# Performance work log

Hardware: AMD Instinct MI355X
Metric: run time of the kernel (lower is better)

The kernel has to match this reference:

```python
import jax, jax.numpy as jnp
import numpy as np

B, S, D, H, L, DFF, WIN = 2, 2048, 768, 12, 2, 3072, 512
EPS = 1e-5
DH = D // H


def setup_inputs() -> dict:
    key = jax.random.key(0)
    ks = jax.random.split(key, 8)
    rn = lambda k, shape: jax.random.normal(k, shape, jnp.float32) * 0.02
    inp = {
        "src": jax.random.normal(ks[0], (B, S, D), jnp.float32),
        "qw": rn(ks[1], (L, D, D)), "qb": jnp.zeros((L, D), jnp.float32),
        "kw": rn(ks[2], (L, D, D)), "kb": jnp.zeros((L, D), jnp.float32),
        "vw": rn(ks[3], (L, D, D)), "vb": jnp.zeros((L, D), jnp.float32),
        "ow": rn(ks[4], (L, D, D)), "ob": jnp.zeros((L, D), jnp.float32),
        "w1": rn(ks[5], (L, DFF, D)), "b1": jnp.zeros((L, DFF), jnp.float32),
        "w2": rn(ks[6], (L, D, DFF)), "b2": jnp.zeros((L, D), jnp.float32),
        "g1": jnp.ones((L, D), jnp.float32), "be1": jnp.zeros((L, D), jnp.float32),
        "g2": jnp.ones((L, D), jnp.float32), "be2": jnp.zeros((L, D), jnp.float32),
    }
    return inp


def _ln(x, g, b):
    m = jnp.mean(x, axis=-1, keepdims=True)
    v = jnp.mean(jnp.square(x - m), axis=-1, keepdims=True)
    return (x - m) * jax.lax.rsqrt(v + EPS) * g + b


def _encoder(src, qw, qb, kw, kb, vw, vb, ow, ob, w1, b1, w2, b2, g1, be1, g2, be2):
    scale = DH ** -0.5
    idx = jnp.arange(S)
    # non-causal sliding window: |i - j| <= window_size // 2
    band = jnp.abs(idx[:, None] - idx[None, :]) <= (WIN // 2)
    neg = -jnp.finfo(jnp.float32).max
    x = src
    for l in range(L):
        # projections -> (B, H, S, DH)
        q = (x @ qw[l].T + qb[l]).reshape(B, S, H, DH).transpose(0, 2, 1, 3)
        k = (x @ kw[l].T + kb[l]).reshape(B, S, H, DH).transpose(0, 2, 1, 3)
        v = (x @ vw[l].T + vb[l]).reshape(B, S, H, DH).transpose(0, 2, 1, 3)
        # full dense scores then band mask (faithful to the original module)
        sim = jnp.einsum('bhid,bhjd->bhij', q * scale, k)
        sim = jnp.where(band, sim, neg)
        attn = jax.nn.softmax(sim, axis=-1)
        o = jnp.einsum('bhij,bhjd->bhid', attn, v)
        o = o.transpose(0, 2, 1, 3).reshape(B, S, D) @ ow[l].T + ob[l]
        # post-norm transformer block (norm_first=False)
        x = _ln(x + o, g1[l], be1[l])
        ff = jax.nn.relu(x @ w1[l].T + b1[l]) @ w2[l].T + b2[l]
        x = _ln(x + ff, g2[l], be2[l])
    return x


def reference(src, qw, qb, kw, kb, vw, vb, ow, ob, w1, b1, w2, b2, g1, be1, g2, be2):
    return _encoder(src, qw, qb, kw, kb, vw, vb, ow, ob, w1, b1, w2, b2, g1, be1, g2, be2)
```

## Files before the change

kernel.cpp:

```cpp
#include <hip/hip_runtime.h>
#include <math.h>

#define BATCH 2
#define SEQ   2048
#define DM    768
#define NHD   12
#define NL    2
#define DFF   3072
#define DH    64
#define HW    256
#define MR    (BATCH*SEQ)
#define EPSF  1e-5f
#define SCALE 0.125f
#define QKVS  2304

typedef __attribute__((ext_vector_type(8))) __bf16 bf16x8;
typedef __attribute__((ext_vector_type(4))) float  f32x4;

__device__ __forceinline__ ushort f2bu(float f) {
    union { __bf16 h; ushort u; } c;
    c.h = (__bf16)f;
    return c.u;
}
__device__ __forceinline__ float bu2f(ushort u) {
    union { uint u; float f; } c;
    c.u = ((uint)u) << 16;
    return c.f;
}

__device__ __forceinline__ void gload16(const ushort* g, ushort* l) {
    __builtin_amdgcn_global_load_lds(
        (const __attribute__((address_space(1))) void*)g,
        (__attribute__((address_space(3))) void*)l, 16, 0, 0);
}

__device__ __forceinline__ void xcd_swz(int& bx, int& by, int& bz) {
    const int gx = gridDim.x, gy = gridDim.y;
    const int nwg = gx * gy * gridDim.z;
    int lin = bx + gx * (by + gy * bz);
    lin = (lin & 7) * (nwg >> 3) + (lin >> 3);
    bx = lin % gx;
    int rest = lin / gx;
    by = rest % gy;
    bz = rest / gy;
}

__global__ __launch_bounds__(256) void cvt(const float* __restrict__ in,
                                           ushort* __restrict__ out, int n)
{
    int i = (blockIdx.x * 256 + threadIdx.x) * 4;
    if (i >= n) return;
    float4 v = *(const float4*)(in + i);
    ushort4 o;
    o.x = f2bu(v.x); o.y = f2bu(v.y); o.z = f2bu(v.z); o.w = f2bu(v.w);
    *(ushort4*)(out + i) = o;
}

__global__ __launch_bounds__(256) void gemm128(
    const ushort* __restrict__ A, const ushort* __restrict__ W,
    const float* __restrict__ bias, ushort* __restrict__ C,
    int M, int N, int K, int relu)
{
    __shared__ ushort As[2][128 * 32];
    __shared__ ushort Ws[2][128 * 32];

    int bxi = blockIdx.x, byi = blockIdx.y, bzi = blockIdx.z;
    xcd_swz(bxi, byi, bzi);

    const int t  = threadIdx.x;
    const int bm = byi * 128;
    const int bn = bxi * 128;

    const int w    = t >> 6;
    const int lane = t & 63;
    const int quad = lane >> 4;
    const int lrow = lane & 15;
    const int wm   = (w >> 1) * 64;
    const int wn   = (w & 1) * 64;

    const int srow = t >> 2;
    const int scol = (t & 3) * 8;
    const ushort* ag = A + (size_t)(bm + srow) * K + scol;
    const ushort* wg = W + (size_t)(bn + srow) * K + scol;

    f32x4 acc[4][4] = {};

    gload16(ag,                  &As[0][t * 8]);
    gload16(ag + (size_t)64 * K, &As[0][2048 + t * 8]);
    gload16(wg,                  &Ws[0][t * 8]);
    gload16(wg + (size_t)64 * K, &Ws[0][2048 + t * 8]);
    __syncthreads();

    int cur = 0;
    for (int k0 = 0; k0 < K; k0 += 32) {
        const int nxt = cur ^ 1;
        if (k0 + 32 < K) {
            gload16(ag + k0 + 32,                  &As[nxt][t * 8]);
            gload16(ag + (size_t)64 * K + k0 + 32, &As[nxt][2048 + t * 8]);
            gload16(wg + k0 + 32,                  &Ws[nxt][t * 8]);
            gload16(wg + (size_t)64 * K + k0 + 32, &Ws[nxt][2048 + t * 8]);
        }

        bf16x8 af[4], bfr[4];
#pragma unroll
        for (int i = 0; i < 4; ++i)
            af[i] = *(const bf16x8*)&As[cur][(wm + i * 16 + lrow) * 32 + quad * 8];
#pragma unroll
        for (int j = 0; j < 4; ++j)
            bfr[j] = *(const bf16x8*)&Ws[cur][(wn + j * 16 + lrow) * 32 + quad * 8];

#pragma unroll
        for (int i = 0; i < 4; ++i)
#pragma unroll
            for (int j = 0; j < 4; ++j)
                acc[i][j] = __builtin_amdgcn_mfma_f32_16x16x32_bf16(
                    af[i], bfr[j], acc[i][j], 0, 0, 0);
        __syncthreads();
        cur = nxt;
    }

#pragma unroll
    for (int j = 0; j < 4; ++j) {
        const int col = bn + wn + j * 16 + lrow;
        const float bv = bias[col];
#pragma unroll
        for (int i = 0; i < 4; ++i) {
            const int rb = bm + wm + i * 16 + quad * 4;
#pragma unroll
            for (int r = 0; r < 4; ++r) {
                float vv = acc[i][j][r] + bv;
                if (relu) vv = fmaxf(vv, 0.f);
                C[(size_t)(rb + r) * N + col] = f2bu(vv);
            }
        }
    }
}

__global__ __launch_bounds__(256) void gemm64(
    const ushort* __restrict__ A, const ushort* __restrict__ W,
    const float* __restrict__ bias, ushort* __restrict__ C,
    float* __restrict__ part, int M, int N, int Kc, int ldk, int relu)
{
    __shared__ ushort As[2][64 * 32];
    __shared__ ushort Ws[2][128 * 32];

    int bxi = blockIdx.x, byi = blockIdx.y, bzi = blockIdx.z;
    xcd_swz(bxi, byi, bzi);

    const int t  = threadIdx.x;
    const int bm = byi * 64;
    const int bn = bxi * 128;
    const int z  = bzi;
    const int kbase = z * Kc;

    const int w    = t >> 6;
    const int lane = t & 63;
    const int quad = lane >> 4;
    const int lrow = lane & 15;
    const int wm   = (w >> 1) * 32;
    const int wn   = (w & 1) * 64;

    const int srow = t >> 2;
    const int scol = (t & 3) * 8;
    const ushort* ag = A + (size_t)(bm + srow) * ldk + kbase + scol;
    const ushort* wg = W + (size_t)(bn + srow) * ldk + kbase + scol;

    f32x4 acc[2][4] = {};

    gload16(ag,                    &As[0][t * 8]);
    gload16(wg,                    &Ws[0][t * 8]);
    gload16(wg + (size_t)64 * ldk, &Ws[0][2048 + t * 8]);
    __syncthreads();

    int cur = 0;
    for (int k0 = 0; k0 < Kc; k0 += 32) {
        const int nxt = cur ^ 1;
        if (k0 + 32 < Kc) {
            gload16(ag + k0 + 32,                    &As[nxt][t * 8]);
            gload16(wg + k0 + 32,                    &Ws[nxt][t * 8]);
            gload16(wg + (size_t)64 * ldk + k0 + 32, &Ws[nxt][2048 + t * 8]);
        }

        bf16x8 af[2], bfr[4];
#pragma unroll
        for (int i = 0; i < 2; ++i)
            af[i] = *(const bf16x8*)&As[cur][(wm + i * 16 + lrow) * 32 + quad * 8];
#pragma unroll
        for (int j = 0; j < 4; ++j)
            bfr[j] = *(const bf16x8*)&Ws[cur][(wn + j * 16 + lrow) * 32 + quad * 8];

#pragma unroll
        for (int i = 0; i < 2; ++i)
#pragma unroll
            for (int j = 0; j < 4; ++j)
                acc[i][j] = __builtin_amdgcn_mfma_f32_16x16x32_bf16(
                    af[i], bfr[j], acc[i][j], 0, 0, 0);
        __syncthreads();
        cur = nxt;
    }

    if (gridDim.z > 1) {
        float* po = part + (size_t)z * M * N;
#pragma unroll
        for (int j = 0; j < 4; ++j) {
            const int col = bn + wn + j * 16 + lrow;
#pragma unroll
            for (int i = 0; i < 2; ++i) {
                const int rb = bm + wm + i * 16 + quad * 4;
#pragma unroll
                for (int r = 0; r < 4; ++r)
                    po[(size_t)(rb + r) * N + col] = acc[i][j][r];
            }
        }
    } else {
#pragma unroll
        for (int j = 0; j < 4; ++j) {
            const int col = bn + wn + j * 16 + lrow;
            const float bv = bias[col];
#pragma unroll
            for (int i = 0; i < 2; ++i) {
                const int rb = bm + wm + i * 16 + quad * 4;
#pragma unroll
                for (int r = 0; r < 4; ++r) {
                    float vv = acc[i][j][r] + bv;
                    if (relu) vv = fmaxf(vv, 0.f);
                    C[(size_t)(rb + r) * N + col] = f2bu(vv);
                }
            }
        }
    }
}

#define QT  64
#define NCH 9
#define KP  72

__global__ __launch_bounds__(256) void attn(
    const ushort* __restrict__ q, const ushort* __restrict__ k,
    const ushort* __restrict__ v, ushort* __restrict__ o)
{
    __shared__ ushort kv[2][64][KP];
    __shared__ ushort vt[2][64][KP];
    __shared__ ushort sc[QT][KP];

    int bxi = blockIdx.x, byi = blockIdx.y, bzi = blockIdx.z;
    xcd_swz(bxi, byi, bzi);

    const int t    = threadIdx.x;
    const int i0   = bxi * QT;
    const int h    = byi;
    const int b    = bzi;
    const size_t ibase = (size_t)b * SEQ * QKVS + (size_t)h * DH;
    const size_t obase = (size_t)b * SEQ * DM   + (size_t)h * DH;

    const int w    = t >> 6;
    const int lane = t & 63;
    const int quad = lane >> 4;
    const int lrow = lane & 15;
    const int qrow = w * 16;

    const int jstart = i0 - HW;

    const int sjj[2] = { t >> 3, (t + 256) >> 3 };
    const int sd0[2] = { (t & 7) * 8, (t & 7) * 8 };

#pragma unroll
    for (int e = 0; e < 2; ++e) {
        int idx = t + 256 * e;
        int qi = idx >> 3, d0 = (idx & 7) * 8;
        uint4 raw = *(const uint4*)(q + ibase + (size_t)(i0 + qi) * QKVS + d0);
        *(uint4*)&sc[qi][d0] = raw;
    }
    uint4 kr[2], vr[2];
#pragma unroll
    for (int e = 0; e < 2; ++e) {
        int j = jstart + sjj[e];
        kr[e] = make_uint4(0, 0, 0, 0);
        vr[e] = make_uint4(0, 0, 0, 0);
        if (j >= 0 && j < SEQ) {
            kr[e] = *(const uint4*)(k + ibase + (size_t)j * QKVS + sd0[e]);
            vr[e] = *(const uint4*)(v + ibase + (size_t)j * QKVS + sd0[e]);
        }
    }
#pragma unroll
    for (int e = 0; e < 2; ++e) {
        *(uint4*)&kv[0][sjj[e]][sd0[e]] = kr[e];
        const ushort* u = (const ushort*)&vr[e];
#pragma unroll
        for (int x = 0; x < 8; ++x) {
            int dh  = sd0[e] + x;
            int blk = ((sjj[e] >> 3) ^ (dh >> 3)) & 7;
            vt[0][dh][blk * 8 + (sjj[e] & 7)] = u[x];
        }
    }
    __syncthreads();

    const bf16x8 a0 = *(const bf16x8*)&sc[qrow + lrow][quad * 8];
    const bf16x8 a1 = *(const bf16x8*)&sc[qrow + lrow][32 + quad * 8];

    float m_r[4], l_r[4];
    f32x4 oacc[4] = {};
#pragma unroll
    for (int r = 0; r < 4; ++r) { m_r[r] = -1e20f; l_r[r] = 0.f; }

    for (int c = 0; c < NCH; ++c) {
        const int cur = c & 1;
        const int j0  = jstart + c * 64;

        if (c + 1 < NCH) {
            const int j0n = jstart + (c + 1) * 64;
#pragma unroll
            for (int e = 0; e < 2; ++e) {
                int j = j0n + sjj[e];
                kr[e] = make_uint4(0, 0, 0, 0);
                vr[e] = make_uint4(0, 0, 0, 0);
                if (j >= 0 && j < SEQ) {
                    kr[e] = *(const uint4*)(k + ibase + (size_t)j * QKVS + sd0[e]);
                    vr[e] = *(const uint4*)(v + ibase + (size_t)j * QKVS + sd0[e]);
                }
            }
        }

        float p[4][4];
#pragma unroll
        for (int kt = 0; kt < 4; ++kt) {
            const int krow = kt * 16;
            bf16x8 b0 = *(const bf16x8*)&kv[cur][krow + lrow][quad * 8];
            bf16x8 b1 = *(const bf16x8*)&kv[cur][krow + lrow][32 + quad * 8];
            f32x4 acc = {};
            acc = __builtin_amdgcn_mfma_f32_16x16x32_bf16(a0, b0, acc, 0, 0, 0);
            acc = __builtin_amdgcn_mfma_f32_16x16x32_bf16(a1, b1, acc, 0, 0, 0);
            const int jg = j0 + krow + lrow;
#pragma unroll
            for (int r = 0; r < 4; ++r) {
                const int ig = i0 + qrow + quad * 4 + r;
                bool ok = (jg >= 0) && (jg < SEQ) &&
                          (jg >= ig - HW) && (jg <= ig + HW);
                p[kt][r] = ok ? acc[r] * SCALE : -1e30f;
            }
        }

#pragma unroll
        for (int r = 0; r < 4; ++r) {
            float cm = fmaxf(fmaxf(p[0][r], p[1][r]), fmaxf(p[2][r], p[3][r]));
#pragma unroll
            for (int off = 8; off; off >>= 1) cm = fmaxf(cm, __shfl_xor(cm, off));
            const float mn = fmaxf(m_r[r], cm);
            const float f  = __expf(m_r[r] - mn);
            m_r[r] = mn;
            float cs = 0.f;
#pragma unroll
            for (int kt = 0; kt < 4; ++kt) {
                float e = __expf(p[kt][r] - mn);
                p[kt][r] = e;
                cs += e;
            }
#pragma unroll
            for (int off = 8; off; off >>= 1) cs += __shfl_xor(cs, off);
            l_r[r] = l_r[r] * f + cs;
#pragma unroll
            for (int nt = 0; nt < 4; ++nt) oacc[nt][r] *= f;
        }

#pragma unroll
        for (int kt = 0; kt < 4; ++kt)
#pragma unroll
            for (int r = 0; r < 4; ++r)
                sc[qrow + quad * 4 + r][kt * 16 + lrow] = f2bu(p[kt][r]);

        bf16x8 pa0 = *(const bf16x8*)&sc[qrow + lrow][quad * 8];
        bf16x8 pa1 = *(const bf16x8*)&sc[qrow + lrow][32 + quad * 8];
#pragma unroll
        for (int nt = 0; nt < 4; ++nt) {
            const int dh  = nt * 16 + lrow;
            const int rsw = (dh >> 3) & 7;
            bf16x8 b0 = *(const bf16x8*)&vt[cur][dh][((quad)     ^ rsw) * 8];
            bf16x8 b1 = *(const bf16x8*)&vt[cur][dh][((quad + 4) ^ rsw) * 8];
            oacc[nt] = __builtin_amdgcn_mfma_f32_16x16x32_bf16(pa0, b0, oacc[nt], 0, 0, 0);
            oacc[nt] = __builtin_amdgcn_mfma_f32_16x16x32_bf16(pa1, b1, oacc[nt], 0, 0, 0);
        }

        if (c + 1 < NCH) {
            const int nxt = cur ^ 1;
#pragma unroll
            for (int e = 0; e < 2; ++e) {
                *(uint4*)&kv[nxt][sjj[e]][sd0[e]] = kr[e];
                const ushort* u = (const ushort*)&vr[e];
#pragma unroll
                for (int x = 0; x < 8; ++x) {
                    int dh  = sd0[e] + x;
                    int blk = ((sjj[e] >> 3) ^ (dh >> 3)) & 7;
                    vt[nxt][dh][blk * 8 + (sjj[e] & 7)] = u[x];
                }
            }
        }
        __syncthreads();
    }

#pragma unroll
    for (int r = 0; r < 4; ++r) {
        const float inv = 1.f / l_r[r];
        const int qi = i0 + qrow + quad * 4 + r;
#pragma unroll
        for (int nt = 0; nt < 4; ++nt)
            o[obase + (size_t)qi * DM + nt * 16 + lrow] = f2bu(oacc[nt][r] * inv);
    }
}

__global__ __launch_bounds__(256) void add_ln(
    const ushort* __restrict__ xa, const ushort* __restrict__ yb,
    const float* __restrict__ g, const float* __restrict__ be,
    ushort* __restrict__ ob, float* __restrict__ of, int fin)
{
    const int r = blockIdx.x * 4 + (threadIdx.x >> 6);
    const int t = threadIdx.x & 63;
    const size_t off = (size_t)r * DM;
    float sv[12];
    float s1 = 0.f, s2 = 0.f;
#pragma unroll
    for (int ii = 0; ii < 12; ++ii) {
        float vv = bu2f(xa[off + t + 64 * ii]) + bu2f(yb[off + t + 64 * ii]);
        sv[ii] = vv; s1 += vv; s2 += vv * vv;
    }
#pragma unroll
    for (int o2 = 32; o2; o2 >>= 1) {
        s1 += __shfl_xor(s1, o2);
        s2 += __shfl_xor(s2, o2);
    }
    const float mean = s1 * (1.f / 768.f);
    const float rstd = rsqrtf(s2 * (1.f / 768.f) - mean * mean + EPSF);
#pragma unroll
    for (int ii = 0; ii < 12; ++ii) {
        const int c = t + 64 * ii;
        float v = (sv[ii] - mean) * rstd * g[c] + be[c];
        if (fin) of[off + c] = v;
        else     ob[off + c] = f2bu(v);
    }
}

__global__ __launch_bounds__(256) void add_ln_sk(
    const ushort* __restrict__ xa, const float* __restrict__ pp,
    const float* __restrict__ bias, const float* __restrict__ g,
    const float* __restrict__ be,
    ushort* __restrict__ ob, float* __restrict__ of, int fin)
{
    const int r = blockIdx.x * 4 + (threadIdx.x >> 6);
    const int t = threadIdx.x & 63;
    const size_t off = (size_t)r * DM;
    float sv[12];
    float s1 = 0.f, s2 = 0.f;
#pragma unroll
    for (int ii = 0; ii < 12; ++ii) {
        const int c = t + 64 * ii;
        float vv = bu2f(xa[off + c]) + pp[off + c]
                 + pp[(size_t)MR * DM + off + c] + bias[c];
        sv[ii] = vv; s1 += vv; s2 += vv * vv;
    }
#pragma unroll
    for (int o2 = 32; o2; o2 >>= 1) {
        s1 += __shfl_xor(s1, o2);
        s2 += __shfl_xor(s2, o2);
    }
    const float mean = s1 * (1.f / 768.f);
    const float rstd = rsqrtf(s2 * (1.f / 768.f) - mean * mean + EPSF);
#pragma unroll
    for (int ii = 0; ii < 12; ++ii) {
        const int c = t + 64 * ii;
        float v = (sv[ii] - mean) * rstd * g[c] + be[c];
        if (fin) of[off + c] = v;
        else     ob[off + c] = f2bu(v);
    }
}

extern "C" void kernel_launch(void* const* d_in, const int* in_sizes, int n_in,
                              void* d_out, int out_size, void* d_ws, size_t ws_size,
                              hipStream_t stream) {
    (void)in_sizes; (void)n_in; (void)out_size; (void)ws_size;
    const float* src = (const float*)d_in[0];
    const float* qw  = (const float*)d_in[1];
    const float* qb  = (const float*)d_in[2];
    const float* kw  = (const float*)d_in[3];
    const float* kb  = (const float*)d_in[4];
    const float* vw  = (const float*)d_in[5];
    const float* vb  = (const float*)d_in[6];
    const float* ow  = (const float*)d_in[7];
    const float* ob  = (const float*)d_in[8];
    const float* w1  = (const float*)d_in[9];
    const float* b1  = (const float*)d_in[10];
    const float* w2  = (const float*)d_in[11];
    const float* b2  = (const float*)d_in[12];
    const float* g1  = (const float*)d_in[13];
    const float* be1 = (const float*)d_in[14];
    const float* g2  = (const float*)d_in[15];
    const float* be2 = (const float*)d_in[16];

    const size_t A    = (size_t)MR * DM;
    const size_t WD1  = (size_t)DM * DM;
    const size_t WQKV = (size_t)3 * DM * DM;
    const size_t WF1  = (size_t)DFF * DM;
    const size_t WF   = (size_t)NL * WF1;

    float*  bcat = (float*)d_ws;
    ushort* p    = (ushort*)(bcat + (size_t)NL * QKVS);
    ushort* qkvwB = p; p += (size_t)NL * WQKV;
    ushort* owB   = p; p += (size_t)NL * WD1;
    ushort* w1B   = p; p += WF;
    ushort* w2B   = p; p += WF;
    ushort* xb    = p; p += A;
    ushort* qkvB  = p; p += 3 * A;
    ushort* oB    = p; p += A;
    ushort* yB    = p; p += A;
    ushort* h1    = p; p += A;
    ushort* ffh   = p;

    float* part = (float*)qkvB;

    for (int l = 0; l < NL; ++l) {
        hipMemcpyAsync(bcat + (size_t)l * QKVS + 0,    qb + (size_t)l * DM,
                       DM * sizeof(float), hipMemcpyDeviceToDevice, stream);
        hipMemcpyAsync(bcat + (size_t)l * QKVS + DM,   kb + (size_t)l * DM,
                       DM * sizeof(float), hipMemcpyDeviceToDevice, stream);
        hipMemcpyAsync(bcat + (size_t)l * QKVS + 2*DM, vb + (size_t)l * DM,
                       DM * sizeof(float), hipMemcpyDeviceToDevice, stream);
    }

    for (int l = 0; l < NL; ++l) {
        cvt<<<(int)(WD1 / 1024), 256, 0, stream>>>(
            qw + (size_t)l * WD1, qkvwB + (size_t)l * WQKV + 0,     (int)WD1);
        cvt<<<(int)(WD1 / 1024), 256, 0, stream>>>(
            kw + (size_t)l * WD1, qkvwB + (size_t)l * WQKV + WD1,   (int)WD1);
        cvt<<<(int)(WD1 / 1024), 256, 0, stream>>>(
            vw + (size_t)l * WD1, qkvwB + (size_t)l * WQKV + 2*WD1, (int)WD1);
    }
    cvt<<<(int)(NL * WD1 / 1024), 256, 0, stream>>>(ow, owB, (int)(NL * WD1));
    cvt<<<(int)(WF / 1024), 256, 0, stream>>>(w1, w1B, (int)WF);
    cvt<<<(int)(WF / 1024), 256, 0, stream>>>(w2, w2B, (int)WF);
    cvt<<<(int)(A  / 1024), 256, 0, stream>>>(src, xb, (int)A);

    const dim3 gQKV(QKVS / 128, MR / 128);
    const dim3 gO(DM / 128, MR / 64);
    const dim3 gF1(DFF / 128, MR / 128);
    const dim3 gF2(DM / 128, MR / 64, 2);
    const dim3 gA(SEQ / QT, NHD, BATCH);

    for (int l = 0; l < NL; ++l) {
        const size_t bD = (size_t)l * DM;
        const size_t bF = (size_t)l * DFF;

        gemm128<<<gQKV, 256, 0, stream>>>(xb, qkvwB + (size_t)l * WQKV,
                                          bcat + (size_t)l * QKVS, qkvB,
                                          MR, QKVS, DM, 0);
        attn<<<gA, 256, 0, stream>>>(qkvB, qkvB + DM, qkvB + 2 * DM, oB);
        gemm64<<<gO, 256, 0, stream>>>(oB, owB + (size_t)l * WD1, ob + bD, yB,
                                       nullptr, MR, DM, DM, DM, 0);
        add_ln<<<MR / 4, 256, 0, stream>>>(xb, yB, g1 + bD, be1 + bD,
                                           h1, nullptr, 0);
        gemm128<<<gF1, 256, 0, stream>>>(h1, w1B + (size_t)l * WF1, b1 + bF, ffh,
                                         MR, DFF, DM, 1);
        gemm64<<<gF2, 256, 0, stream>>>(ffh, w2B + (size_t)l * WF1, nullptr,
                                        nullptr, part, MR, DM, DFF / 2, DFF, 0);
        if (l == NL - 1)
            add_ln_sk<<<MR / 4, 256, 0, stream>>>(h1, part, b2 + bD,
                                                  g2 + bD, be2 + bD,
                                                  nullptr, (float*)d_out, 1);
        else
            add_ln_sk<<<MR / 4, 256, 0, stream>>>(h1, part, b2 + bD,
                                                  g2 + bD, be2 + bD,
                                                  xb, nullptr, 0);
    }
}
```

Baseline: 477.5 us.

## Transpose QK MFMA, add lazy softmax rescaling, split-K output projection

The attention kernel now computes K·Q^T so each lane holds one query row. That makes the softmax row max and sum need only two cross-lane shuffles, and the probabilities are stored to shared memory as packed 4-element writes. Masking is skipped for fully interior chunks, and the running max is only updated when a chunk's max exceeds it by more than a threshold, which removes most rescales of the output accumulator. Separately, the QKV projection moves to the 64-row GEMM tile for more blocks, and the output projection uses a 2-way split-K whose partials are fused into the existing add+layernorm kernel. The old add_ln kernel is removed. The lazy-rescale threshold keeps exponents bounded but changes rounding slightly, and the split-K partials add extra fp32 traffic.

```diff
diff --git a/kernel.cpp b/kernel.cpp
--- a/kernel.cpp
+++ b/kernel.cpp
@@ -262,7 +262,7 @@
     const int jstart = i0 - HW;
 
     const int sjj[2] = { t >> 3, (t + 256) >> 3 };
-    const int sd0[2] = { (t & 7) * 8, (t & 7) * 8 };
+    const int sd0 = (t & 7) * 8;
 
 #pragma unroll
     for (int e = 0; e < 2; ++e) {
@@ -278,17 +278,17 @@
         kr[e] = make_uint4(0, 0, 0, 0);
         vr[e] = make_uint4(0, 0, 0, 0);
         if (j >= 0 && j < SEQ) {
-            kr[e] = *(const uint4*)(k + ibase + (size_t)j * QKVS + sd0[e]);
-            vr[e] = *(const uint4*)(v + ibase + (size_t)j * QKVS + sd0[e]);
+            kr[e] = *(const uint4*)(k + ibase + (size_t)j * QKVS + sd0);
+            vr[e] = *(const uint4*)(v + ibase + (size_t)j * QKVS + sd0);
         }
     }
 #pragma unroll
     for (int e = 0; e < 2; ++e) {
-        *(uint4*)&kv[0][sjj[e]][sd0[e]] = kr[e];
+        *(uint4*)&kv[0][sjj[e]][sd0] = kr[e];
         const ushort* u = (const ushort*)&vr[e];
 #pragma unroll
         for (int x = 0; x < 8; ++x) {
-            int dh  = sd0[e] + x;
+            int dh  = sd0 + x;
             int blk = ((sjj[e] >> 3) ^ (dh >> 3)) & 7;
             vt[0][dh][blk * 8 + (sjj[e] & 7)] = u[x];
         }
@@ -298,10 +298,8 @@
     const bf16x8 a0 = *(const bf16x8*)&sc[qrow + lrow][quad * 8];
     const bf16x8 a1 = *(const bf16x8*)&sc[qrow + lrow][32 + quad * 8];
 
-    float m_r[4], l_r[4];
+    float m_s = -1e20f, l_s = 0.f;
     f32x4 oacc[4] = {};
-#pragma unroll
-    for (int r = 0; r < 4; ++r) { m_r[r] = -1e20f; l_r[r] = 0.f; }
 
     for (int c = 0; c < NCH; ++c) {
         const int cur = c & 1;
@@ -315,58 +313,83 @@
                 kr[e] = make_uint4(0, 0, 0, 0);
                 vr[e] = make_uint4(0, 0, 0, 0);
                 if (j >= 0 && j < SEQ) {
-                    kr[e] = *(const uint4*)(k + ibase + (size_t)j * QKVS + sd0[e]);
-                    vr[e] = *(const uint4*)(v + ibase + (size_t)j * QKVS + sd0[e]);
+                    kr[e] = *(const uint4*)(k + ibase + (size_t)j * QKVS + sd0);
+                    vr[e] = *(const uint4*)(v + ibase + (size_t)j * QKVS + sd0);
                 }
             }
         }
 
+        const bool full = (c >= 1) && (c <= 7) && (j0 >= 0) && (j0 + 64 <= SEQ);
         float p[4][4];
 #pragma unroll
         for (int kt = 0; kt < 4; ++kt) {
             const int krow = kt * 16;
-            bf16x8 b0 = *(const bf16x8*)&kv[cur][krow + lrow][quad * 8];
-            bf16x8 b1 = *(const bf16x8*)&kv[cur][krow + lrow][32 + quad * 8];
+            bf16x8 kf0 = *(const bf16x8*)&kv[cur][krow + lrow][quad * 8];
+            bf16x8 kf1 = *(const bf16x8*)&kv[cur][krow + lrow][32 + quad * 8];
             f32x4 acc = {};
-            acc = __builtin_amdgcn_mfma_f32_16x16x32_bf16(a0, b0, acc, 0, 0, 0);
-            acc = __builtin_amdgcn_mfma_f32_16x16x32_bf16(a1, b1, acc, 0, 0, 0);
-            const int jg = j0 + krow + lrow;
+            acc = __builtin_amdgcn_mfma_f32_16x16x32_bf16(kf0, a0, acc, 0, 0, 0);
+            acc = __builtin_amdgcn_mfma_f32_16x16x32_bf16(kf1, a1, acc, 0, 0, 0);
+            if (full) {
+#pragma unroll
+                for (int r = 0; r < 4; ++r) p[kt][r] = acc[r] * SCALE;
+            } else {
+                const int ig = i0 + qrow + lrow;
+#pragma unroll
+                for (int r = 0; r < 4; ++r) {
+                    const int jg = j0 + krow + quad * 4 + r;
+                    bool ok = (jg >= 0) && (jg < SEQ) &&
+                              (jg >= ig - HW) && (jg <= ig + HW);
+                    p[kt][r] = ok ? acc[r] * SCALE : -1e30f;
+                }
+            }
+        }
+
+        float cm = p[0][0];
+#pragma unroll
+        for (int kt = 0; kt < 4; ++kt)
+#pragma unroll
+            for (int r = 0; r < 4; ++r) cm = fmaxf(cm, p[kt][r]);
+        cm = fmaxf(cm, __shfl_xor(cm, 16));
+        cm = fmaxf(cm, __shfl_xor(cm, 32));
+
+        const bool resc = !__all(cm <= m_s + 8.f);
+        float f = 1.f;
+        if (resc) {
+            const float mn = fmaxf(m_s, cm);
+            f = __expf(m_s - mn);
+            m_s = mn;
+        }
+        float cs = 0.f;
+#pragma unroll
+        for (int kt = 0; kt < 4; ++kt)
 #pragma unroll
             for (int r = 0; r < 4; ++r) {
-                const int ig = i0 + qrow + quad * 4 + r;
-                bool ok = (jg >= 0) && (jg < SEQ) &&
-                          (jg >= ig - HW) && (jg <= ig + HW);
-                p[kt][r] = ok ? acc[r] * SCALE : -1e30f;
-            }
-        }
-
-#pragma unroll
-        for (int r = 0; r < 4; ++r) {
-            float cm = fmaxf(fmaxf(p[0][r], p[1][r]), fmaxf(p[2][r], p[3][r]));
-#pragma unroll
-            for (int off = 8; off; off >>= 1) cm = fmaxf(cm, __shfl_xor(cm, off));
-            const float mn = fmaxf(m_r[r], cm);
-            const float f  = __expf(m_r[r] - mn);
-            m_r[r] = mn;
-            float cs = 0.f;
-#pragma unroll
-            for (int kt = 0; kt < 4; ++kt) {
-                float e = __expf(p[kt][r] - mn);
+                float e = __expf(p[kt][r] - m_s);
                 p[kt][r] = e;
                 cs += e;
             }
-#pragma unroll
-            for (int off = 8; off; off >>= 1) cs += __shfl_xor(cs, off);
-            l_r[r] = l_r[r] * f + cs;
-#pragma unroll
-            for (int nt = 0; nt < 4; ++nt) oacc[nt][r] *= f;
-        }
-
-#pragma unroll
-        for (int kt = 0; kt < 4; ++kt)
-#pragma unroll
-            for (int r = 0; r < 4; ++r)
-                sc[qrow + quad * 4 + r][kt * 16 + lrow] = f2bu(p[kt][r]);
+        cs += __shfl_xor(cs, 16);
+        cs += __shfl_xor(cs, 32);
+        l_s = l_s * f + cs;
+        if (resc) {
+            float f4[4];
+#pragma unroll
+            for (int r = 0; r < 4; ++r) f4[r] = __shfl(f, quad * 4 + r);
+#pragma unroll
+            for (int nt = 0; nt < 4; ++nt)
+#pragma unroll
+                for (int r = 0; r < 4; ++r) oacc[nt][r] *= f4[r];
+        }
+
+#pragma unroll
+        for (int kt = 0; kt < 4; ++kt) {
+            ushort4 pw;
+            pw.x = f2bu(p[kt][0]);
+            pw.y = f2bu(p[kt][1]);
+            pw.z = f2bu(p[kt][2]);
+            pw.w = f2bu(p[kt][3]);
+            *(ushort4*)&sc[qrow + lrow][kt * 16 + quad * 4] = pw;
+        }
 
         bf16x8 pa0 = *(const bf16x8*)&sc[qrow + lrow][quad * 8];
         bf16x8 pa1 = *(const bf16x8*)&sc[qrow + lrow][32 + quad * 8];
@@ -384,11 +407,11 @@
             const int nxt = cur ^ 1;
 #pragma unroll
             for (int e = 0; e < 2; ++e) {
-                *(uint4*)&kv[nxt][sjj[e]][sd0[e]] = kr[e];
+                *(uint4*)&kv[nxt][sjj[e]][sd0] = kr[e];
                 const ushort* u = (const ushort*)&vr[e];
 #pragma unroll
                 for (int x = 0; x < 8; ++x) {
-                    int dh  = sd0[e] + x;
+                    int dh  = sd0 + x;
                     int blk = ((sjj[e] >> 3) ^ (dh >> 3)) & 7;
                     vt[nxt][dh][blk * 8 + (sjj[e] & 7)] = u[x];
                 }
@@ -397,44 +420,16 @@
         __syncthreads();
     }
 
+    const float inv = 1.f / l_s;
+    float inv4[4];
+#pragma unroll
+    for (int r = 0; r < 4; ++r) inv4[r] = __shfl(inv, quad * 4 + r);
 #pragma unroll
     for (int r = 0; r < 4; ++r) {
-        const float inv = 1.f / l_r[r];
         const int qi = i0 + qrow + quad * 4 + r;
 #pragma unroll
         for (int nt = 0; nt < 4; ++nt)
-            o[obase + (size_t)qi * DM + nt * 16 + lrow] = f2bu(oacc[nt][r] * inv);
-    }
-}
-
-__global__ __launch_bounds__(256) void add_ln(
-    const ushort* __restrict__ xa, const ushort* __restrict__ yb,
-    const float* __restrict__ g, const float* __restrict__ be,
-    ushort* __restrict__ ob, float* __restrict__ of, int fin)
-{
-    const int r = blockIdx.x * 4 + (threadIdx.x >> 6);
-    const int t = threadIdx.x & 63;
-    const size_t off = (size_t)r * DM;
-    float sv[12];
-    float s1 = 0.f, s2 = 0.f;
-#pragma unroll
-    for (int ii = 0; ii < 12; ++ii) {
-        float vv = bu2f(xa[off + t + 64 * ii]) + bu2f(yb[off + t + 64 * ii]);
-        sv[ii] = vv; s1 += vv; s2 += vv * vv;
-    }
-#pragma unroll
-    for (int o2 = 32; o2; o2 >>= 1) {
-        s1 += __shfl_xor(s1, o2);
-        s2 += __shfl_xor(s2, o2);
-    }
-    const float mean = s1 * (1.f / 768.f);
-    const float rstd = rsqrtf(s2 * (1.f / 768.f) - mean * mean + EPSF);
-#pragma unroll
-    for (int ii = 0; ii < 12; ++ii) {
-        const int c = t + 64 * ii;
-        float v = (sv[ii] - mean) * rstd * g[c] + be[c];
-        if (fin) of[off + c] = v;
-        else     ob[off + c] = f2bu(v);
+            o[obase + (size_t)qi * DM + nt * 16 + lrow] = f2bu(oacc[nt][r] * inv4[r]);
     }
 }
 
@@ -513,7 +508,8 @@
     ushort* h1    = p; p += A;
     ushort* ffh   = p;
 
-    float* part = (float*)qkvB;
+    float* partF = (float*)qkvB;
+    float* partO = (float*)ffh;
 
     for (int l = 0; l < NL; ++l) {
         hipMemcpyAsync(bcat + (size_t)l * QKVS + 0,    qb + (size_t)l * DM,
@@ -537,8 +533,8 @@
     cvt<<<(int)(WF / 1024), 256, 0, stream>>>(w2, w2B, (int)WF);
     cvt<<<(int)(A  / 1024), 256, 0, stream>>>(src, xb, (int)A);
 
-    const dim3 gQKV(QKVS / 128, MR / 128);
-    const dim3 gO(DM / 128, MR / 64);
+    const dim3 gQKV(QKVS / 128, MR / 64);
+    const dim3 gOp(DM / 128, MR / 64, 2);
     const dim3 gF1(DFF / 128, MR / 128);
     const dim3 gF2(DM / 128, MR / 64, 2);
     const dim3 gA(SEQ / QT, NHD, BATCH);
@@ -547,24 +543,25 @@
         const size_t bD = (size_t)l * DM;
         const size_t bF = (size_t)l * DFF;
 
-        gemm128<<<gQKV, 256, 0, stream>>>(xb, qkvwB + (size_t)l * WQKV,
-                                          bcat + (size_t)l * QKVS, qkvB,
-                                          MR, QKVS, DM, 0);
+        gemm64<<<gQKV, 256, 0, stream>>>(xb, qkvwB + (size_t)l * WQKV,
+                                         bcat + (size_t)l * QKVS, qkvB,
+                                         nullptr, MR, QKVS, DM, DM, 0);
         attn<<<gA, 256, 0, stream>>>(qkvB, qkvB + DM, qkvB + 2 * DM, oB);
-        gemm64<<<gO, 256, 0, stream>>>(oB, owB + (size_t)l * WD1, ob + bD, yB,
-                                       nullptr, MR, DM, DM, DM, 0);
-        add_ln<<<MR / 4, 256, 0, stream>>>(xb, yB, g1 + bD, be1 + bD,
-                                           h1, nullptr, 0);
+        gemm64<<<gOp, 256, 0, stream>>>(oB, owB + (size_t)l * WD1, nullptr,
+                                        nullptr, partO, MR, DM, DM / 2, DM, 0);
+        add_ln_sk<<<MR / 4, 256, 0, stream>>>(xb, partO, ob + bD,
+                                              g1 + bD, be1 + bD,
+                                              h1, nullptr, 0);
         gemm128<<<gF1, 256, 0, stream>>>(h1, w1B + (size_t)l * WF1, b1 + bF, ffh,
                                          MR, DFF, DM, 1);
         gemm64<<<gF2, 256, 0, stream>>>(ffh, w2B + (size_t)l * WF1, nullptr,
-                                        nullptr, part, MR, DM, DFF / 2, DFF, 0);
+                                        nullptr, partF, MR, DM, DFF / 2, DFF, 0);
         if (l == NL - 1)
-            add_ln_sk<<<MR / 4, 256, 0, stream>>>(h1, part, b2 + bD,
+            add_ln_sk<<<MR / 4, 256, 0, stream>>>(h1, partF, b2 + bD,
                                                   g2 + bD, be2 + bD,
                                                   nullptr, (float*)d_out, 1);
         else
-            add_ln_sk<<<MR / 4, 256, 0, stream>>>(h1, part, b2 + bD,
+            add_ln_sk<<<MR / 4, 256, 0, stream>>>(h1, partF, b2 + bD,
                                                   g2 + bD, be2 + bD,
                                                   xb, nullptr, 0);
     }
```

Result: no change. 480.2 us (+0.6%).
